# Optimization experiments

Measured on AMD Instinct MI355X. Metric: run time of the kernel, lower is better.

Reference implementation:

```python
import jax, jax.numpy as jnp
import numpy as np

EMBED_DIM = 1024
NUM_HEADS = 16
HEAD_DIM = EMBED_DIM // NUM_HEADS
SCALE = HEAD_DIM ** -0.5


def setup_inputs() -> dict:
    key = jax.random.key(0)
    k1, k2, k3 = jax.random.split(key, 3)
    B, S, E = 2, 2048, EMBED_DIM
    # xavier-uniform-like init scaled down for stability
    x = jax.random.normal(k1, (B, S, E), dtype=jnp.float32)
    w_qkv = jax.random.normal(k2, (3 * E, E), dtype=jnp.float32) * (E ** -0.5)
    w_out = jax.random.normal(k3, (E, E), dtype=jnp.float32) * (E ** -0.5)
    bias_qkv = jnp.zeros((3 * E,), dtype=jnp.float32)
    bias_out = jnp.zeros((E,), dtype=jnp.float32)
    return {"x": x, "w_qkv": w_qkv, "bias_qkv": bias_qkv, "w_out": w_out, "bias_out": bias_out}


def reference(x, w_qkv, bias_qkv, w_out, bias_out):
    B, S, E = x.shape
    H, D = NUM_HEADS, HEAD_DIM
    # fused QKV projection: nn.Linear semantics -> x @ w_qkv.T + bias
    qkv = jnp.einsum('bse,fe->bsf', x, w_qkv) + bias_qkv  # [B,S,3E]
    q, k, v = jnp.split(qkv, 3, axis=-1)
    # reshape to heads
    q = q.reshape(B, S, H, D)
    k = k.reshape(B, S, H, D)
    v = v.reshape(B, S, H, D)
    # scaled dot-product attention (non-causal)
    scores = jnp.einsum('bqhd,bkhd->bhqk', q, k) * SCALE  # [B,H,S,S]
    probs = jax.nn.softmax(scores, axis=-1)
    ctx = jnp.einsum('bhqk,bkhd->bqhd', probs, v).reshape(B, S, E)
    # output projection
    out = jnp.einsum('bse,fe->bsf', ctx, w_out) + bias_out
    return out
```

## Files before the change

### kernel.cpp

```cpp
#include <hip/hip_runtime.h>
#include <hip/hip_bf16.h>


typedef __bf16 bf16_t;
typedef __bf16 bf16x4 __attribute__((ext_vector_type(4)));
typedef __bf16 bf16x8 __attribute__((ext_vector_type(8)));
typedef float f32x4 __attribute__((ext_vector_type(4)));

#define MFMA16(a, b, c) __builtin_amdgcn_mfma_f32_16x16x32_bf16(a, b, c, 0, 0, 0)

static constexpr int Bn = 2;
static constexpr int S = 2048;
static constexpr int E = 1024;
static constexpr int H = 16;
static constexpr int Dh = 64;

__device__ __forceinline__ void gl_lds16(const bf16_t* g, bf16_t* l) {
  __builtin_amdgcn_global_load_lds(
      (const __attribute__((address_space(1))) unsigned int*)g,
      (__attribute__((address_space(3))) unsigned int*)l, 16, 0, 0);
}

__device__ __forceinline__ int detect_fp32(const unsigned short* p) {
  int cnt = 0;
#pragma unroll
  for (int j = 0; j < 32; j++) {
    const int e = (p[j] >> 7) & 0xFF;
    cnt += (e > 140) ? 1 : 0;
  }
  return cnt >= 2;
}

static constexpr int G0 = 4194304 / 8;
static constexpr int G1 = G0 + 3145728 / 8;
static constexpr int G2 = G1 + 3072 / 8;
static constexpr int G3 = G2 + 1048576 / 8;
static constexpr int G4 = G3 + 1024 / 8;

__global__ void convert_all(const void* __restrict__ s0, const void* __restrict__ s1,
                            const void* __restrict__ s2, const void* __restrict__ s3,
                            const void* __restrict__ s4, bf16_t* __restrict__ dst) {
  const int fp32 = detect_fp32((const unsigned short*)s0);
  const int stride = gridDim.x * blockDim.x;
  for (int i = blockIdx.x * blockDim.x + threadIdx.x; i < G4; i += stride) {
    const void* s;
    int off;
    if (i < G0)      { s = s0; off = i; }
    else if (i < G1) { s = s1; off = i - G0; }
    else if (i < G2) { s = s2; off = i - G1; }
    else if (i < G3) { s = s3; off = i - G2; }
    else             { s = s4; off = i - G3; }
    bf16x8 o;
    if (fp32) {
      const float* sp = (const float*)s + off * 8;
#pragma unroll
      for (int j = 0; j < 8; j++) o[j] = (bf16_t)sp[j];
    } else {
      o = *((const bf16x8*)s + off);
    }
    *(bf16x8*)(dst + (size_t)i * 8) = o;
  }
}

__global__ __launch_bounds__(256) void gemm_qkv(
    const bf16_t* __restrict__ X, const bf16_t* __restrict__ W,
    const bf16_t* __restrict__ bias,
    bf16_t* __restrict__ Qo, bf16_t* __restrict__ Ko, bf16_t* __restrict__ Vo) {
  __shared__ bf16_t Alds[16 * 512];
  __shared__ bf16_t Blds[16 * 512];
  const int tid = threadIdx.x;
  const int wave = tid >> 6, lane = tid & 63;
  const int lr = lane & 15, quad = lane >> 4;
  const int wm = wave >> 1, wn = wave & 1;
  const int m0 = blockIdx.y * 128, n0 = blockIdx.x * 128;
  constexpr int Kd = 1024;

  f32x4 acc[4][4] = {};
  for (int k0 = 0; k0 < Kd; k0 += 64) {
    __syncthreads();
#pragma unroll
    for (int i = 0; i < 4; i++) {
      const int fb = wave * 4 + i;
      const int mt = fb >> 1, kc = fb & 1;
      gl_lds16(X + (size_t)(m0 + mt * 16 + lr) * Kd + k0 + kc * 32 + quad * 8,
               &Alds[fb * 512]);
      gl_lds16(W + (size_t)(n0 + mt * 16 + lr) * Kd + k0 + kc * 32 + quad * 8,
               &Blds[fb * 512]);
    }
    __syncthreads();
#pragma unroll
    for (int kc = 0; kc < 2; kc++) {
      bf16x8 af[4], bfr[4];
#pragma unroll
      for (int mt = 0; mt < 4; mt++)
        af[mt] = *(const bf16x8*)&Alds[((wm * 4 + mt) * 2 + kc) * 512 + lane * 8];
#pragma unroll
      for (int nt = 0; nt < 4; nt++)
        bfr[nt] = *(const bf16x8*)&Blds[((wn * 4 + nt) * 2 + kc) * 512 + lane * 8];
#pragma unroll
      for (int mt = 0; mt < 4; mt++)
#pragma unroll
        for (int nt = 0; nt < 4; nt++)
          acc[mt][nt] = MFMA16(af[mt], bfr[nt], acc[mt][nt]);
    }
  }

  const int m0w = m0 + wm * 64, n0w = n0 + wn * 64;
#pragma unroll
  for (int nt = 0; nt < 4; nt++) {
    const int col = n0w + nt * 16 + lr;
    const float bs = (float)bias[col];
    const int which = col >> 10;
    const int e = col & 1023;
    const int h = e >> 6, d = e & 63;
#pragma unroll
    for (int mt = 0; mt < 4; mt++) {
      const int row0 = m0w + mt * 16 + quad * 4;
      const int b = row0 >> 11, s0 = row0 & 2047;
      if (which == 2) {
        bf16x4 v4;
#pragma unroll
        for (int r = 0; r < 4; r++) v4[r] = (bf16_t)(acc[mt][nt][r] + bs);
        *(bf16x4*)&Vo[((size_t)((b * H + h) * Dh + d)) * S + s0] = v4;
      } else {
        bf16_t* dst = (which == 0) ? Qo : Ko;
#pragma unroll
        for (int r = 0; r < 4; r++)
          dst[((size_t)((b * H + h) * S + (s0 + r))) * Dh + d] =
              (bf16_t)(acc[mt][nt][r] + bs);
      }
    }
  }
}

__global__ __launch_bounds__(256, 4) void attn_kernel(
    const bf16_t* __restrict__ Q, const bf16_t* __restrict__ K,
    const bf16_t* __restrict__ Vt, bf16_t* __restrict__ CTX) {
  constexpr int LDP = 72;
  __shared__ bf16_t Kl[8 * 512];
  __shared__ bf16_t Vl[8 * 512];
  __shared__ bf16_t Psh[4 * 16 * LDP];

  const int tid = threadIdx.x;
  const int wave = tid >> 6, lane = tid & 63;
  const int lr = lane & 15, quad = lane >> 4;

  const int blk = blockIdx.x;
  const int bh = blk & 31;
  const int qt = blk >> 5;
  const int b = bh >> 4, h = bh & 15;

  const bf16_t* Qb = Q + (size_t)bh * S * Dh;
  const bf16_t* Kb = K + (size_t)bh * S * Dh;
  const bf16_t* Vb = Vt + (size_t)bh * Dh * S;

  const int q0 = qt * 64 + wave * 16;

  const bf16x8 aq0 = *(const bf16x8*)(Qb + (size_t)(q0 + lr) * Dh + quad * 8);
  const bf16x8 aq1 = *(const bf16x8*)(Qb + (size_t)(q0 + lr) * Dh + 32 + quad * 8);

  bf16x8 ones;
#pragma unroll
  for (int j = 0; j < 8; j++) ones[j] = (bf16_t)1.0f;

  bf16_t* pw = &Psh[wave * 16 * LDP];

  const bf16_t* kg = Kb + (size_t)(wave * 16 + lr) * Dh + quad * 8;
  const bf16_t* vg = Vb + (size_t)(wave * 16 + lr) * S + quad * 8;

  f32x4 O[4] = {};
  f32x4 lacc = {};

  for (int sk0 = 0; sk0 < S; sk0 += 64) {
    __syncthreads();
    gl_lds16(kg + (size_t)sk0 * Dh, &Kl[(wave * 2 + 0) * 512]);
    gl_lds16(kg + (size_t)sk0 * Dh + 32, &Kl[(wave * 2 + 1) * 512]);
    gl_lds16(vg + sk0, &Vl[(wave * 2 + 0) * 512]);
    gl_lds16(vg + sk0 + 32, &Vl[(wave * 2 + 1) * 512]);
    __syncthreads();

    f32x4 sc[4];
#pragma unroll
    for (int nt = 0; nt < 4; nt++) {
      const bf16x8 k0f = *(const bf16x8*)&Kl[(nt * 2 + 0) * 512 + lane * 8];
      const bf16x8 k1f = *(const bf16x8*)&Kl[(nt * 2 + 1) * 512 + lane * 8];
      f32x4 z = {};
      z = MFMA16(aq0, k0f, z);
      sc[nt] = MFMA16(aq1, k1f, z);
    }

    bf16x8 vf[4][2];
#pragma unroll
    for (int dt = 0; dt < 4; dt++) {
      vf[dt][0] = *(const bf16x8*)&Vl[(dt * 2 + 0) * 512 + lane * 8];
      vf[dt][1] = *(const bf16x8*)&Vl[(dt * 2 + 1) * 512 + lane * 8];
    }

#pragma unroll
    for (int nt = 0; nt < 4; nt++)
#pragma unroll
      for (int r = 0; r < 4; r++) {
        const float p = __expf(sc[nt][r] * 0.125f);
        pw[(quad * 4 + r) * LDP + nt * 16 + lr] = (bf16_t)p;
      }

    const bf16x8 ap0 = *(const bf16x8*)(&pw[lr * LDP + quad * 8]);
    const bf16x8 ap1 = *(const bf16x8*)(&pw[lr * LDP + 32 + quad * 8]);
    lacc = MFMA16(ap0, ones, lacc);
    lacc = MFMA16(ap1, ones, lacc);
#pragma unroll
    for (int dt = 0; dt < 4; dt++) {
      O[dt] = MFMA16(ap0, vf[dt][0], O[dt]);
      O[dt] = MFMA16(ap1, vf[dt][1], O[dt]);
    }
  }

  float rl[4];
#pragma unroll
  for (int r = 0; r < 4; r++) rl[r] = 1.0f / lacc[r];
#pragma unroll
  for (int dt = 0; dt < 4; dt++)
#pragma unroll
    for (int r = 0; r < 4; r++) {
      const int qrow = q0 + quad * 4 + r;
      CTX[(size_t)(b * S + qrow) * E + h * 64 + dt * 16 + lr] =
          (bf16_t)(O[dt][r] * rl[r]);
    }
}

__global__ __launch_bounds__(256) void gemm_out(
    const bf16_t* __restrict__ X, const bf16_t* __restrict__ W,
    const bf16_t* __restrict__ bias, void* __restrict__ Out,
    const void* __restrict__ xin) {
  __shared__ bf16_t Alds[8 * 512];
  __shared__ bf16_t Blds[16 * 512];
  const int tid = threadIdx.x;
  const int wave = tid >> 6, lane = tid & 63;
  const int lr = lane & 15, quad = lane >> 4;
  const int wm = wave >> 1, wn = wave & 1;
  const int m0 = blockIdx.y * 64, n0 = blockIdx.x * 128;
  constexpr int Kd = 1024;

  f32x4 acc[2][4] = {};
  for (int k0 = 0; k0 < Kd; k0 += 64) {
    __syncthreads();
#pragma unroll
    for (int kc = 0; kc < 2; kc++)
      gl_lds16(X + (size_t)(m0 + wave * 16 + lr) * Kd + k0 + kc * 32 + quad * 8,
               &Alds[(wave * 2 + kc) * 512]);
#pragma unroll
    for (int i = 0; i < 2; i++) {
      const int nt = wave * 2 + i;
#pragma unroll
      for (int kc = 0; kc < 2; kc++)
        gl_lds16(W + (size_t)(n0 + nt * 16 + lr) * Kd + k0 + kc * 32 + quad * 8,
                 &Blds[(nt * 2 + kc) * 512]);
    }
    __syncthreads();
#pragma unroll
    for (int kc = 0; kc < 2; kc++) {
      bf16x8 af[2], bfr[4];
#pragma unroll
      for (int mt = 0; mt < 2; mt++)
        af[mt] = *(const bf16x8*)&Alds[((wm * 2 + mt) * 2 + kc) * 512 + lane * 8];
#pragma unroll
      for (int nt = 0; nt < 4; nt++)
        bfr[nt] = *(const bf16x8*)&Blds[((wn * 4 + nt) * 2 + kc) * 512 + lane * 8];
#pragma unroll
      for (int mt = 0; mt < 2; mt++)
#pragma unroll
        for (int nt = 0; nt < 4; nt++)
          acc[mt][nt] = MFMA16(af[mt], bfr[nt], acc[mt][nt]);
    }
  }

  const int fp32 = detect_fp32((const unsigned short*)xin);
  const int m0w = m0 + wm * 32, n0w = n0 + wn * 64;
#pragma unroll
  for (int nt = 0; nt < 4; nt++) {
    const int col = n0w + nt * 16 + lr;
    const float bs = (float)bias[col];
#pragma unroll
    for (int mt = 0; mt < 2; mt++) {
#pragma unroll
      for (int r = 0; r < 4; r++) {
        const int row = m0w + mt * 16 + quad * 4 + r;
        const float v = acc[mt][nt][r] + bs;
        if (fp32)
          ((float*)Out)[(size_t)row * E + col] = v;
        else
          ((bf16_t*)Out)[(size_t)row * E + col] = (bf16_t)v;
      }
    }
  }
}

extern "C" void kernel_launch(void* const* d_in, const int* in_sizes, int n_in,
                              void* d_out, int out_size, void* d_ws, size_t ws_size,
                              hipStream_t stream) {
  const void* x = d_in[0];
  const void* w_qkv = d_in[1];
  const void* b_qkv = d_in[2];
  const void* w_out = d_in[3];
  const void* b_out = d_in[4];

  bf16_t* base = (bf16_t*)d_ws;
  const int N_X = Bn * S * E;
  const int N_WQ = 3 * E * E;
  const int N_BQ = 3 * E;
  const int N_WO = E * E;
  const int N_BO = E;
  bf16_t* xb = base;
  bf16_t* wqb = xb + N_X;
  bf16_t* bqb = wqb + N_WQ;
  bf16_t* wob = bqb + N_BQ;
  bf16_t* bob = wob + N_WO;
  const size_t QKV_ELEMS = (size_t)Bn * H * S * Dh;
  bf16_t* Qw = bob + N_BO;
  bf16_t* Kw = Qw + QKV_ELEMS;
  bf16_t* Vw = Kw + QKV_ELEMS;
  bf16_t* CTXw = Vw + QKV_ELEMS;

  convert_all<<<1024, 256, 0, stream>>>(x, w_qkv, b_qkv, w_out, b_out, xb);
  gemm_qkv<<<dim3(3 * E / 128, Bn * S / 128), 256, 0, stream>>>(xb, wqb, bqb, Qw, Kw, Vw);
  attn_kernel<<<32 * Bn * H, 256, 0, stream>>>(Qw, Kw, Vw, CTXw);
  gemm_out<<<dim3(E / 128, Bn * S / 64), 256, 0, stream>>>(CTXw, wob, bob, d_out, x);
}
```

Measured before the change: 227.0 us.

## Double-buffer K/V tiles in attention, fold scale into Q, swizzle P buffer

Result: no change. 229.4 us (+1.1%).

```diff
diff --git a/kernel.cpp b/kernel.cpp
--- a/kernel.cpp
+++ b/kernel.cpp
@@ -136,10 +136,9 @@
 __global__ __launch_bounds__(256, 4) void attn_kernel(
     const bf16_t* __restrict__ Q, const bf16_t* __restrict__ K,
     const bf16_t* __restrict__ Vt, bf16_t* __restrict__ CTX) {
-  constexpr int LDP = 72;
-  __shared__ bf16_t Kl[8 * 512];
-  __shared__ bf16_t Vl[8 * 512];
-  __shared__ bf16_t Psh[4 * 16 * LDP];
+  __shared__ bf16_t Kl[2 * 8 * 512];
+  __shared__ bf16_t Vl[2 * 8 * 512];
+  __shared__ bf16_t Psh[4 * 16 * 64];
 
   const int tid = threadIdx.x;
   const int wave = tid >> 6, lane = tid & 63;
@@ -156,14 +155,20 @@
 
   const int q0 = qt * 64 + wave * 16;
 
-  const bf16x8 aq0 = *(const bf16x8*)(Qb + (size_t)(q0 + lr) * Dh + quad * 8);
-  const bf16x8 aq1 = *(const bf16x8*)(Qb + (size_t)(q0 + lr) * Dh + 32 + quad * 8);
+  bf16x8 aq0 = *(const bf16x8*)(Qb + (size_t)(q0 + lr) * Dh + quad * 8);
+  bf16x8 aq1 = *(const bf16x8*)(Qb + (size_t)(q0 + lr) * Dh + 32 + quad * 8);
+#pragma unroll
+  for (int j = 0; j < 8; j++) {
+    aq0[j] = (bf16_t)((float)aq0[j] * 0.125f);
+    aq1[j] = (bf16_t)((float)aq1[j] * 0.125f);
+  }
 
   bf16x8 ones;
 #pragma unroll
   for (int j = 0; j < 8; j++) ones[j] = (bf16_t)1.0f;
 
-  bf16_t* pw = &Psh[wave * 16 * LDP];
+  bf16_t* pw = &Psh[wave * 16 * 64];
+  const int xl = (lr & 7) << 3;
 
   const bf16_t* kg = Kb + (size_t)(wave * 16 + lr) * Dh + quad * 8;
   const bf16_t* vg = Vb + (size_t)(wave * 16 + lr) * S + quad * 8;
@@ -171,19 +176,33 @@
   f32x4 O[4] = {};
   f32x4 lacc = {};
 
+  {
+    gl_lds16(kg, &Kl[(wave * 2 + 0) * 512]);
+    gl_lds16(kg + 32, &Kl[(wave * 2 + 1) * 512]);
+    gl_lds16(vg, &Vl[(wave * 2 + 0) * 512]);
+    gl_lds16(vg + 32, &Vl[(wave * 2 + 1) * 512]);
+  }
+  __syncthreads();
+
+  int buf = 0;
+#pragma unroll 2
   for (int sk0 = 0; sk0 < S; sk0 += 64) {
-    __syncthreads();
-    gl_lds16(kg + (size_t)sk0 * Dh, &Kl[(wave * 2 + 0) * 512]);
-    gl_lds16(kg + (size_t)sk0 * Dh + 32, &Kl[(wave * 2 + 1) * 512]);
-    gl_lds16(vg + sk0, &Vl[(wave * 2 + 0) * 512]);
-    gl_lds16(vg + sk0 + 32, &Vl[(wave * 2 + 1) * 512]);
-    __syncthreads();
+    const int bb = buf * 4096;
+    const int nb = (buf ^ 1) * 4096;
+
+    if (sk0 + 64 < S) {
+      const int skn = sk0 + 64;
+      gl_lds16(kg + (size_t)skn * Dh, &Kl[nb + (wave * 2 + 0) * 512]);
+      gl_lds16(kg + (size_t)skn * Dh + 32, &Kl[nb + (wave * 2 + 1) * 512]);
+      gl_lds16(vg + skn, &Vl[nb + (wave * 2 + 0) * 512]);
+      gl_lds16(vg + skn + 32, &Vl[nb + (wave * 2 + 1) * 512]);
+    }
 
     f32x4 sc[4];
 #pragma unroll
     for (int nt = 0; nt < 4; nt++) {
-      const bf16x8 k0f = *(const bf16x8*)&Kl[(nt * 2 + 0) * 512 + lane * 8];
-      const bf16x8 k1f = *(const bf16x8*)&Kl[(nt * 2 + 1) * 512 + lane * 8];
+      const bf16x8 k0f = *(const bf16x8*)&Kl[bb + (nt * 2 + 0) * 512 + lane * 8];
+      const bf16x8 k1f = *(const bf16x8*)&Kl[bb + (nt * 2 + 1) * 512 + lane * 8];
       f32x4 z = {};
       z = MFMA16(aq0, k0f, z);
       sc[nt] = MFMA16(aq1, k1f, z);
@@ -192,20 +211,21 @@
     bf16x8 vf[4][2];
 #pragma unroll
     for (int dt = 0; dt < 4; dt++) {
-      vf[dt][0] = *(const bf16x8*)&Vl[(dt * 2 + 0) * 512 + lane * 8];
-      vf[dt][1] = *(const bf16x8*)&Vl[(dt * 2 + 1) * 512 + lane * 8];
+      vf[dt][0] = *(const bf16x8*)&Vl[bb + (dt * 2 + 0) * 512 + lane * 8];
+      vf[dt][1] = *(const bf16x8*)&Vl[bb + (dt * 2 + 1) * 512 + lane * 8];
     }
 
 #pragma unroll
     for (int nt = 0; nt < 4; nt++)
 #pragma unroll
       for (int r = 0; r < 4; r++) {
-        const float p = __expf(sc[nt][r] * 0.125f);
-        pw[(quad * 4 + r) * LDP + nt * 16 + lr] = (bf16_t)p;
+        const float p = __expf(sc[nt][r]);
+        const int qr = quad * 4 + r;
+        pw[qr * 64 + ((nt * 16 + lr) ^ ((qr & 7) << 3))] = (bf16_t)p;
       }
 
-    const bf16x8 ap0 = *(const bf16x8*)(&pw[lr * LDP + quad * 8]);
-    const bf16x8 ap1 = *(const bf16x8*)(&pw[lr * LDP + 32 + quad * 8]);
+    const bf16x8 ap0 = *(const bf16x8*)&pw[lr * 64 + ((quad * 8) ^ xl)];
+    const bf16x8 ap1 = *(const bf16x8*)&pw[lr * 64 + ((quad * 8 + 32) ^ xl)];
     lacc = MFMA16(ap0, ones, lacc);
     lacc = MFMA16(ap1, ones, lacc);
 #pragma unroll
@@ -213,6 +233,9 @@
       O[dt] = MFMA16(ap0, vf[dt][0], O[dt]);
       O[dt] = MFMA16(ap1, vf[dt][1], O[dt]);
     }
+
+    __syncthreads();
+    buf ^= 1;
   }
 
   float rl[4];
```
